# Kernel tuning notes

Measured on AMD Instinct MI355X. Metric: run time of the kernel, lower is better.

The kernel has to match this reference:

```python
import jax, jax.numpy as jnp
import numpy as np

B, S, D, N, L, V = 2, 512, 1024, 4096, 4, 32000
EPS = 1e-5

def ternarize(w):
    # BitNet b1.58-style: scale = mean |w|, quantize to {-1,0,1}, rescale.
    s = jnp.mean(jnp.abs(w)) + 1e-8
    return s * jnp.round(jnp.clip(w / s, -1.0, 1.0))

def tern_ste(w):
    # straight-through estimator (faithful to ternary training)
    return w + jax.lax.stop_gradient(ternarize(w) - w)

def layer_norm(x, g, b):
    mu = jnp.mean(x, axis=-1, keepdims=True)
    var = jnp.var(x, axis=-1, keepdims=True)
    return (x - mu) * jax.lax.rsqrt(var + EPS) * g + b

def setup_inputs() -> dict:
    key = jax.random.key(0)
    ks = jax.random.split(key, 20)
    sc = lambda d: 1.0 / np.sqrt(d)
    inp = {
        'input_ids': jax.random.randint(ks[0], (B, S), 0, V, dtype=jnp.int32),
        'emb':       jax.random.normal(ks[1], (V, D), jnp.float32) * 0.02,
        'pos_emb':   jax.random.normal(ks[2], (S, D), jnp.float32) * 0.02,
        'gru_wih':   jax.random.normal(ks[3], (3 * D, D), jnp.float32) * sc(D),
        'gru_whh':   jax.random.normal(ks[4], (3 * D, D), jnp.float32) * sc(D),
        'gru_bih':   jnp.zeros((3 * D,), jnp.float32),
        'gru_bhh':   jnp.zeros((3 * D,), jnp.float32),
        'syn_w':     jax.random.normal(ks[5], (L, N, D), jnp.float32) * sc(D),
        'syn_b':     jnp.zeros((L, N), jnp.float32),
        'out_w':     jax.random.normal(ks[6], (L, D, N), jnp.float32) * sc(N),
        'out_b':     jnp.zeros((L, D), jnp.float32),
        'ln_g':      jnp.ones((L, D), jnp.float32),
        'ln_b':      jnp.zeros((L, D), jnp.float32),
        'on_g':      jnp.ones((D,), jnp.float32),
        'on_b':      jnp.zeros((D,), jnp.float32),
        'head_w':    jax.random.normal(ks[7], (V, D), jnp.float32) * sc(D),
        'head_b':    jnp.zeros((V,), jnp.float32),
    }
    return inp

def gru(x, wih, whh, bih, bhh):
    # x: [B,S,D] -> [B,S,D], torch nn.GRU semantics, h0 = 0
    # Precompute input projections for all timesteps: [B,S,3D]
    gi_all = jnp.einsum('bsd,ed->bse', x, wih) + bih
    def step(h, gi):
        gh = h @ whh.T + bhh
        ir, iz, inn = jnp.split(gi, 3, axis=-1)
        hr, hz, hn = jnp.split(gh, 3, axis=-1)
        r = jax.nn.sigmoid(ir + hr)
        z = jax.nn.sigmoid(iz + hz)
        n = jnp.tanh(inn + r * hn)
        h_new = (1.0 - z) * n + z * h
        return h_new, h_new
    h0 = jnp.zeros((x.shape[0], whh.shape[1]), x.dtype)
    _, hs = jax.lax.scan(step, h0, jnp.swapaxes(gi_all, 0, 1))
    return jnp.swapaxes(hs, 0, 1)

def reference(input_ids, emb, pos_emb, gru_wih, gru_whh, gru_bih, gru_bhh,
              syn_w, syn_b, out_w, out_b, ln_g, ln_b, on_g, on_b,
              head_w, head_b):
    # Ternary embedding lookup
    x = tern_ste(emb)[input_ids]                       # [B,S,D]
    x = x + pos_emb[None, :x.shape[1], :]
    x = gru(x, gru_wih, gru_whh, gru_bih, gru_bhh)
    for l in range(L):
        residual = x
        hidden = jax.nn.relu(jnp.einsum('bsd,nd->bsn', x, tern_ste(syn_w[l])) + syn_b[l])
        out = jnp.einsum('bsn,dn->bsd', hidden, tern_ste(out_w[l])) + out_b[l]
        x = layer_norm(residual + out, ln_g[l], ln_b[l])
    x = layer_norm(x, on_g, on_b)
    logits = jnp.einsum('bsd,vd->bsv', x, tern_ste(head_w)) + head_b  # [B,S,V]
    return logits
```

## Files before the change

kernel.cpp:

```cpp
#include <hip/hip_runtime.h>
#include <hip/hip_bf16.h>
#include <cstdint>
#include <cstddef>

#define Dm 1024
#define Sm 512
#define Bm 2
#define Nm 4096
#define Lm 4
#define Vm 32000

typedef __attribute__((ext_vector_type(8))) short short8;
typedef __attribute__((ext_vector_type(4))) float floatx4;

__device__ __forceinline__ unsigned short f2b(float f){
  union { float f; unsigned u; } v; v.f = f;
  unsigned r = (v.u + 0x7fffu + ((v.u >> 16) & 1u)) >> 16;
  return (unsigned short)r;
}
__device__ __forceinline__ float b2f(unsigned short h){
  union { unsigned u; float f; } v; v.u = ((unsigned)h) << 16;
  return v.f;
}

__device__ __forceinline__ void gload16(const unsigned short* g, unsigned short* l){
  __builtin_amdgcn_global_load_lds(
      (const __attribute__((address_space(1))) void*)g,
      (__attribute__((address_space(3))) void*)l, 16, 0, 0);
}

__global__ __launch_bounds__(256) void absum_all_kernel(
    const float* __restrict__ emb, const float* __restrict__ syn_w,
    const float* __restrict__ out_w, const float* __restrict__ head_w,
    double* __restrict__ partial)
{
  int wid = blockIdx.x >> 7;
  int blk = blockIdx.x & 127;
  const float* base; long n4;
  if (wid == 0){ base = emb; n4 = (long)Vm * Dm / 4; }
  else if (wid <= 4){ base = syn_w + (size_t)(wid - 1) * Nm * Dm; n4 = (long)Nm * Dm / 4; }
  else if (wid <= 8){ base = out_w + (size_t)(wid - 5) * Dm * Nm; n4 = (long)Nm * Dm / 4; }
  else { base = head_w; n4 = (long)Vm * Dm / 4; }

  long i = (long)blk * 256 + threadIdx.x;
  const long stride = 128L * 256;
  double s = 0.0;
  for (; i < n4; i += stride){
    float4 v = ((const float4*)base)[i];
    s += (double)fabsf(v.x) + (double)fabsf(v.y) + (double)fabsf(v.z) + (double)fabsf(v.w);
  }
  #pragma unroll
  for (int off = 32; off; off >>= 1) s += __shfl_down(s, off, 64);
  __shared__ double wsum[4];
  int lane = threadIdx.x & 63, wv = threadIdx.x >> 6;
  if (lane == 0) wsum[wv] = s;
  __syncthreads();
  if (threadIdx.x == 0) partial[wid * 128 + blk] = wsum[0] + wsum[1] + wsum[2] + wsum[3];
}

__global__ __launch_bounds__(128) void scale_kernel(const double* __restrict__ partials,
                                                    float* __restrict__ scales){
  int b = blockIdx.x;
  int tid = threadIdx.x;
  __shared__ double red[128];
  red[tid] = partials[b * 128 + tid];
  __syncthreads();
  for (int off = 64; off; off >>= 1){
    if (tid < off) red[tid] += red[tid + off];
    __syncthreads();
  }
  if (tid == 0){
    double cnt = (b == 0 || b == 9) ? (double)Vm * (double)Dm : (double)Nm * (double)Dm;
    scales[b] = (float)(red[0] / cnt);
  }
}

__global__ __launch_bounds__(256) void tern_kernel(const float* __restrict__ w,
                                                   const float* __restrict__ smean,
                                                   unsigned short* __restrict__ out, long n4){
  float s = smean[0] + 1e-8f;
  long i = (long)blockIdx.x * blockDim.x + threadIdx.x;
  long stride = (long)gridDim.x * blockDim.x;
  for (; i < n4; i += stride){
    float4 v = ((const float4*)w)[i];
    ushort4 o;
    o.x = f2b(rintf(fminf(fmaxf(v.x / s, -1.f), 1.f)));
    o.y = f2b(rintf(fminf(fmaxf(v.y / s, -1.f), 1.f)));
    o.z = f2b(rintf(fminf(fmaxf(v.z / s, -1.f), 1.f)));
    o.w = f2b(rintf(fminf(fmaxf(v.w / s, -1.f), 1.f)));
    ((ushort4*)out)[i] = o;
  }
}

__global__ __launch_bounds__(256) void split_kernel(const float* __restrict__ w,
                                                    unsigned short* __restrict__ hi,
                                                    unsigned short* __restrict__ lo, long n4){
  long i = (long)blockIdx.x * blockDim.x + threadIdx.x;
  long stride = (long)gridDim.x * blockDim.x;
  for (; i < n4; i += stride){
    float4 v = ((const float4*)w)[i];
    float f[4] = {v.x, v.y, v.z, v.w};
    ushort4 h4, l4;
    unsigned short* hp = (unsigned short*)&h4;
    unsigned short* lp = (unsigned short*)&l4;
    #pragma unroll
    for (int e = 0; e < 4; e++){
      unsigned short h = f2b(f[e]);
      hp[e] = h;
      lp[e] = f2b(f[e] - b2f(h));
    }
    ((ushort4*)hi)[i] = h4;
    ((ushort4*)lo)[i] = l4;
  }
}

__global__ __launch_bounds__(256) void embed_kernel(
    const int* __restrict__ ids, const float* __restrict__ emb,
    const float* __restrict__ pos, const float* __restrict__ smean,
    unsigned short* __restrict__ xhi, unsigned short* __restrict__ xlo)
{
  int row = blockIdx.x;
  int sp  = row & (Sm - 1);
  int id  = ids[row];
  float s = smean[0] + 1e-8f;
  int d = threadIdx.x * 4;
  float4 wv = *(const float4*)(emb + (size_t)id * Dm + d);
  float4 pv = *(const float4*)(pos + (size_t)sp * Dm + d);
  float y[4];
  y[0] = s * rintf(fminf(fmaxf(wv.x / s, -1.f), 1.f)) + pv.x;
  y[1] = s * rintf(fminf(fmaxf(wv.y / s, -1.f), 1.f)) + pv.y;
  y[2] = s * rintf(fminf(fmaxf(wv.z / s, -1.f), 1.f)) + pv.z;
  y[3] = s * rintf(fminf(fmaxf(wv.w / s, -1.f), 1.f)) + pv.w;
  ushort4 h4, l4;
  unsigned short* hp = (unsigned short*)&h4;
  unsigned short* lp = (unsigned short*)&l4;
  #pragma unroll
  for (int e = 0; e < 4; e++){
    unsigned short h = f2b(y[e]);
    hp[e] = h;
    lp[e] = f2b(y[e] - b2f(h));
  }
  size_t base = (size_t)row * Dm + d;
  *(ushort4*)(xhi + base) = h4;
  *(ushort4*)(xlo + base) = l4;
}

template<bool WSPLIT, bool WF32, int BT>
__global__ __launch_bounds__(256) void gemm_kernel(
    const unsigned short* __restrict__ Ahi, const unsigned short* __restrict__ Alo,
    const void* __restrict__ Wsrc, const unsigned short* __restrict__ Wlo,
    const float* __restrict__ bias, const float* __restrict__ smean,
    int relu, float* __restrict__ outf,
    unsigned short* __restrict__ outhi, unsigned short* __restrict__ outlo,
    int M, int N, int K)
{
  constexpr int WT = BT / 2;
  constexpr int FT = WT / 16;
  constexpr int RPT = 256 / BT;
  constexpr int CPT = 32 / RPT;
  constexpr int NU  = CPT / 8;

  __shared__ unsigned short As[2][BT][40];
  __shared__ unsigned short Bs[WSPLIT ? 2 : 1][BT][40];
  int tid = threadIdx.x;
  int wave = tid >> 6, lane = tid & 63;
  int wm = wave >> 1, wn = wave & 1;
  int bm = blockIdx.y, bn = blockIdx.x;

  bool tern = (smean != nullptr);
  float s = 1.f;
  if (tern) s = smean[0] + 1e-8f;

  int arow = tid / RPT, sub = tid % RPT;
  int col0 = sub * CPT;
  const unsigned short* Agh = Ahi + (size_t)(bm * BT + arow) * K + col0;
  const unsigned short* Agl = Alo + (size_t)(bm * BT + arow) * K + col0;
  const float* Wgf = nullptr;
  const unsigned short* Wgh = nullptr;
  const unsigned short* Wgl = nullptr;
  if (WF32) Wgf = (const float*)Wsrc + (size_t)(bn * BT + arow) * K + col0;
  else {
    Wgh = (const unsigned short*)Wsrc + (size_t)(bn * BT + arow) * K + col0;
    if (WSPLIT) Wgl = Wlo + (size_t)(bn * BT + arow) * K + col0;
  }

  floatx4 acc[FT][FT];
  #pragma unroll
  for (int i = 0; i < FT; i++)
    #pragma unroll
    for (int j = 0; j < FT; j++)
      acc[i][j] = (floatx4){0.f, 0.f, 0.f, 0.f};

  int kpb = K / (int)gridDim.z;
  int k_beg = blockIdx.z * kpb;

  for (int k0 = k_beg; k0 < k_beg + kpb; k0 += 32){
    __syncthreads();
    #pragma unroll
    for (int u = 0; u < NU; u++){
      *(uint4*)&As[0][arow][col0 + u * 8] = *(const uint4*)(Agh + k0 + u * 8);
      *(uint4*)&As[1][arow][col0 + u * 8] = *(const uint4*)(Agl + k0 + u * 8);
    }
    if (WF32){
      unsigned short tmp[CPT];
      #pragma unroll
      for (int q = 0; q < CPT / 4; q++){
        float4 wv = *(const float4*)(Wgf + k0 + q * 4);
        float f[4] = {wv.x, wv.y, wv.z, wv.w};
        #pragma unroll
        for (int e = 0; e < 4; e++){
          float w = f[e];
          if (tern) w = rintf(fminf(fmaxf(w / s, -1.f), 1.f));
          tmp[q * 4 + e] = f2b(w);
        }
      }
      #pragma unroll
      for (int u = 0; u < NU; u++)
        *(uint4*)&Bs[0][arow][col0 + u * 8] = *(uint4*)&tmp[u * 8];
    } else {
      #pragma unroll
      for (int u = 0; u < NU; u++){
        *(uint4*)&Bs[0][arow][col0 + u * 8] = *(const uint4*)(Wgh + k0 + u * 8);
        if (WSPLIT)
          *(uint4*)&Bs[1][arow][col0 + u * 8] = *(const uint4*)(Wgl + k0 + u * 8);
      }
    }
    __syncthreads();

    int kq = lane >> 4, mr = lane & 15;
    short8 afh[FT], afl[FT], bfh[FT];
    #pragma unroll
    for (int i = 0; i < FT; i++){
      afh[i] = *(const short8*)&As[0][wm*WT + i*16 + mr][kq*8];
      afl[i] = *(const short8*)&As[1][wm*WT + i*16 + mr][kq*8];
    }
    #pragma unroll
    for (int j = 0; j < FT; j++) bfh[j] = *(const short8*)&Bs[0][wn*WT + j*16 + mr][kq*8];
    #pragma unroll
    for (int i = 0; i < FT; i++)
      #pragma unroll
      for (int j = 0; j < FT; j++){
        acc[i][j] = __builtin_amdgcn_mfma_f32_16x16x32_bf16(afh[i], bfh[j], acc[i][j], 0, 0, 0);
        acc[i][j] = __builtin_amdgcn_mfma_f32_16x16x32_bf16(afl[i], bfh[j], acc[i][j], 0, 0, 0);
      }
    if (WSPLIT){
      short8 bfl[FT];
      #pragma unroll
      for (int j = 0; j < FT; j++) bfl[j] = *(const short8*)&Bs[1][wn*WT + j*16 + mr][kq*8];
      #pragma unroll
      for (int i = 0; i < FT; i++)
        #pragma unroll
        for (int j = 0; j < FT; j++)
          acc[i][j] = __builtin_amdgcn_mfma_f32_16x16x32_bf16(afh[i], bfl[j], acc[i][j], 0, 0, 0);
    }
  }

  bool split = (gridDim.z > 1);
  bool addb = (blockIdx.z == 0);
  int cr = lane >> 4, cc = lane & 15;
  #pragma unroll
  for (int j = 0; j < FT; j++){
    int col = bn * BT + wn * WT + j * 16 + cc;
    float bv = (bias && addb) ? bias[col] : 0.f;
    #pragma unroll
    for (int i = 0; i < FT; i++){
      #pragma unroll
      for (int r = 0; r < 4; r++){
        int row = bm * BT + wm * WT + i * 16 + cr * 4 + r;
        float v = acc[i][j][r] * s + bv;
        if (relu) v = fmaxf(v, 0.f);
        size_t idx = (size_t)row * N + col;
        if (outf){
          if (split) atomicAdd(outf + idx, v);
          else outf[idx] = v;
        }
        if (outhi){
          unsigned short h = f2b(v);
          outhi[idx] = h;
          outlo[idx] = f2b(v - b2f(h));
        }
      }
    }
  }
}

__global__ __launch_bounds__(256) void gemm_lds_kernel(
    const unsigned short* __restrict__ Ahi, const unsigned short* __restrict__ Alo,
    const unsigned short* __restrict__ Whi,
    const float* __restrict__ bias, const float* __restrict__ smean,
    int relu, float* __restrict__ outf, int M, int N, int K)
{
  __shared__ __align__(16) unsigned short lds[3 * 4096];
  int tid = threadIdx.x;
  int wave = tid >> 6, lane = tid & 63;
  int wm = wave >> 1, wn = wave & 1;
  int bm = blockIdx.y, bn = blockIdx.x;

  float s = 1.f;
  if (smean) s = smean[0] + 1e-8f;

  int r0 = wave * 32 + (lane >> 2);
  int r1 = r0 + 16;
  int s0 = (lane & 3) ^ ((r0 >> 1) & 3);
  int s1 = (lane & 3) ^ ((r1 >> 1) & 3);
  const unsigned short* ga0 = Ahi + (size_t)(bm * 128 + r0) * K + s0 * 8;
  const unsigned short* ga1 = Ahi + (size_t)(bm * 128 + r1) * K + s1 * 8;
  const unsigned short* gl0 = Alo + (size_t)(bm * 128 + r0) * K + s0 * 8;
  const unsigned short* gl1 = Alo + (size_t)(bm * 128 + r1) * K + s1 * 8;
  const unsigned short* gw0 = Whi + (size_t)(bn * 128 + r0) * K + s0 * 8;
  const unsigned short* gw1 = Whi + (size_t)(bn * 128 + r1) * K + s1 * 8;
  unsigned short* la = &lds[wave * 1024];

  floatx4 acc[4][4];
  #pragma unroll
  for (int i = 0; i < 4; i++)
    #pragma unroll
    for (int j = 0; j < 4; j++)
      acc[i][j] = (floatx4){0.f, 0.f, 0.f, 0.f};

  for (int k0 = 0; k0 < K; k0 += 32){
    __syncthreads();
    gload16(ga0 + k0, la);
    gload16(ga1 + k0, la + 512);
    gload16(gl0 + k0, la + 4096);
    gload16(gl1 + k0, la + 4096 + 512);
    gload16(gw0 + k0, la + 8192);
    gload16(gw1 + k0, la + 8192 + 512);
    __syncthreads();

    int kq = lane >> 4, mr = lane & 15;
    short8 afh[4], afl[4], bfh[4];
    #pragma unroll
    for (int i = 0; i < 4; i++){
      int r = wm * 64 + i * 16 + mr;
      int off = r * 32 + ((kq ^ ((r >> 1) & 3)) << 3);
      afh[i] = *(const short8*)&lds[off];
      afl[i] = *(const short8*)&lds[4096 + off];
    }
    #pragma unroll
    for (int j = 0; j < 4; j++){
      int r = wn * 64 + j * 16 + mr;
      int off = r * 32 + ((kq ^ ((r >> 1) & 3)) << 3);
      bfh[j] = *(const short8*)&lds[8192 + off];
    }
    #pragma unroll
    for (int i = 0; i < 4; i++)
      #pragma unroll
      for (int j = 0; j < 4; j++){
        acc[i][j] = __builtin_amdgcn_mfma_f32_16x16x32_bf16(afh[i], bfh[j], acc[i][j], 0, 0, 0);
        acc[i][j] = __builtin_amdgcn_mfma_f32_16x16x32_bf16(afl[i], bfh[j], acc[i][j], 0, 0, 0);
      }
  }

  int cr = lane >> 4, cc = lane & 15;
  #pragma unroll
  for (int j = 0; j < 4; j++){
    int col = bn * 128 + wn * 64 + j * 16 + cc;
    float bv = bias ? bias[col] : 0.f;
    #pragma unroll
    for (int i = 0; i < 4; i++){
      #pragma unroll
      for (int r = 0; r < 4; r++){
        int row = bm * 128 + wm * 64 + i * 16 + cr * 4 + r;
        float v = acc[i][j][r] * s + bv;
        if (relu) v = fmaxf(v, 0.f);
        outf[(size_t)row * N + col] = v;
      }
    }
  }
}

__global__ __launch_bounds__(1024) void gru_kernel(
    const float* __restrict__ gi, const float* __restrict__ whh, const float* __restrict__ bhh,
    unsigned long long* __restrict__ hbuf, float* __restrict__ hs,
    unsigned short* __restrict__ xhi, unsigned short* __restrict__ xlo)
{
  __shared__ float lds_h[2 * 1088];
  __shared__ float lds_gh[96];
  int w = blockIdx.x, tid = threadIdx.x;
  int d0 = w * 16;
  int o = tid >> 4, c = tid & 15;
  bool active = (o < 48);
  int g = o >> 4, dl = o & 15;
  int wrow = g * Dm + d0 + dl;
  float wreg[64];
  if (active){
    const float* src = whh + (size_t)wrow * Dm + c * 64;
    #pragma unroll
    for (int i = 0; i < 64; i++) wreg[i] = src[i];
  }
  float bhval = active ? bhh[wrow] : 0.f;

  int bb = tid >> 4, dd = tid & 15;
  float hprev = 0.f;

  for (int t = 0; t < Sm; t++){
    float ir = 0.f, iz = 0.f, inn = 0.f;
    if (tid < 32){
      const float* girow = gi + ((size_t)bb * Sm + t) * (3 * Dm);
      int d = d0 + dd;
      ir  = girow[d];
      iz  = girow[Dm + d];
      inn = girow[2 * Dm + d];
    }
    {
      const unsigned long long* src = hbuf + (size_t)(t & 1) * 2048 + tid * 2;
      unsigned got = 0;
      int spins = 0;
      while (got != 3u){
        #pragma unroll
        for (int q = 0; q < 2; q++){
          if (!(got & (1u << q))){
            unsigned long long wd = __hip_atomic_load(src + q, __ATOMIC_RELAXED,
                                                      __HIP_MEMORY_SCOPE_AGENT);
            if ((unsigned)(wd >> 32) == (unsigned)t){
              union { unsigned u; float f; } cv; cv.u = (unsigned)wd;
              int wi = tid * 2 + q;
              int b = wi >> 10, d = wi & 1023;
              lds_h[b * 1088 + (d >> 6) * 68 + (d & 63)] = cv.f;
              got |= 1u << q;
            }
          }
        }
        if (got != 3u){
          if (++spins > (1 << 20)) break;
          __builtin_amdgcn_s_sleep(1);
        }
      }
    }
    __syncthreads();
    if (active){
      const float* hp = lds_h + c * 68;
      float a0 = 0.f, a1 = 0.f;
      #pragma unroll
      for (int i = 0; i < 64; i++){
        float wv = wreg[i];
        a0 += wv * hp[i];
        a1 += wv * hp[1088 + i];
      }
      #pragma unroll
      for (int off = 8; off; off >>= 1){
        a0 += __shfl_xor(a0, off, 16);
        a1 += __shfl_xor(a1, off, 16);
      }
      if (c == 0){
        lds_gh[o]      = a0 + bhval;
        lds_gh[48 + o] = a1 + bhval;
      }
    }
    __syncthreads();
    if (tid < 32){
      float gr = lds_gh[bb * 48 + dd];
      float gz = lds_gh[bb * 48 + 16 + dd];
      float gn = lds_gh[bb * 48 + 32 + dd];
      float rr = 1.f / (1.f + expf(-(ir + gr)));
      float zz = 1.f / (1.f + expf(-(iz + gz)));
      float nn = tanhf(inn + rr * gn);
      float hnew = (1.f - zz) * nn + zz * hprev;
      hprev = hnew;
      int d = d0 + dd;
      union { float f; unsigned u; } cv; cv.f = hnew;
      unsigned long long wd = ((unsigned long long)(unsigned)(t + 1) << 32) | (unsigned long long)cv.u;
      __hip_atomic_store(hbuf + (size_t)((t + 1) & 1) * 2048 + bb * Dm + d, wd,
                         __ATOMIC_RELAXED, __HIP_MEMORY_SCOPE_AGENT);
      size_t oi = ((size_t)bb * Sm + t) * Dm + d;
      hs[oi] = hnew;
      unsigned short h = f2b(hnew);
      xhi[oi] = h;
      xlo[oi] = f2b(hnew - b2f(h));
    }
  }
}

__global__ __launch_bounds__(256) void ln_kernel(
    const float* __restrict__ resid, const float* __restrict__ addv,
    const float* __restrict__ g, const float* __restrict__ b,
    float* __restrict__ outf, unsigned short* __restrict__ outhi,
    unsigned short* __restrict__ outlo)
{
  int row = blockIdx.x;
  int d = threadIdx.x * 4;
  size_t base = (size_t)row * Dm + d;
  float4 v = *(const float4*)(resid + base);
  if (addv){
    float4 a = *(const float4*)(addv + base);
    v.x += a.x; v.y += a.y; v.z += a.z; v.w += a.w;
  }
  float sum = v.x + v.y + v.z + v.w;
  float sq  = v.x*v.x + v.y*v.y + v.z*v.z + v.w*v.w;
  #pragma unroll
  for (int off = 32; off; off >>= 1){
    sum += __shfl_down(sum, off, 64);
    sq  += __shfl_down(sq,  off, 64);
  }
  __shared__ float red[4][2];
  __shared__ float bc[2];
  int lane = threadIdx.x & 63, wv = threadIdx.x >> 6;
  if (lane == 0){ red[wv][0] = sum; red[wv][1] = sq; }
  __syncthreads();
  if (threadIdx.x == 0){
    float st = red[0][0] + red[1][0] + red[2][0] + red[3][0];
    float qt = red[0][1] + red[1][1] + red[2][1] + red[3][1];
    float mu = st * (1.f / Dm);
    float var = qt * (1.f / Dm) - mu * mu;
    bc[0] = mu; bc[1] = rsqrtf(var + 1e-5f);
  }
  __syncthreads();
  float mu = bc[0], rs = bc[1];
  float4 gv = *(const float4*)(g + d);
  float4 bv = *(const float4*)(b + d);
  float y[4];
  y[0] = (v.x - mu) * rs * gv.x + bv.x;
  y[1] = (v.y - mu) * rs * gv.y + bv.y;
  y[2] = (v.z - mu) * rs * gv.z + bv.z;
  y[3] = (v.w - mu) * rs * gv.w + bv.w;
  if (outf) *(float4*)(outf + base) = *(float4*)y;
  if (outhi){
    ushort4 h4, l4;
    unsigned short* hp = (unsigned short*)&h4;
    unsigned short* lp = (unsigned short*)&l4;
    #pragma unroll
    for (int e = 0; e < 4; e++){
      unsigned short h = f2b(y[e]);
      hp[e] = h;
      lp[e] = f2b(y[e] - b2f(h));
    }
    *(ushort4*)(outhi + base) = h4;
    *(ushort4*)(outlo + base) = l4;
  }
}

extern "C" void kernel_launch(void* const* d_in, const int* in_sizes, int n_in,
                              void* d_out, int out_size, void* d_ws, size_t ws_size,
                              hipStream_t stream)
{
  const int*   ids    = (const int*)  d_in[0];
  const float* emb    = (const float*)d_in[1];
  const float* pos    = (const float*)d_in[2];
  const float* wih    = (const float*)d_in[3];
  const float* whh    = (const float*)d_in[4];
  const float* bih    = (const float*)d_in[5];
  const float* bhh    = (const float*)d_in[6];
  const float* syn_w  = (const float*)d_in[7];
  const float* syn_b  = (const float*)d_in[8];
  const float* out_w  = (const float*)d_in[9];
  const float* out_b  = (const float*)d_in[10];
  const float* ln_g   = (const float*)d_in[11];
  const float* ln_b   = (const float*)d_in[12];
  const float* on_g   = (const float*)d_in[13];
  const float* on_b   = (const float*)d_in[14];
  const float* head_w = (const float*)d_in[15];
  const float* head_b = (const float*)d_in[16];
  float* logits = (float*)d_out;

  const size_t MB = (size_t)1 << 20;
  char* ws = (char*)d_ws;
  float*  scales   = (float*) ws;
  double* partials = (double*)(ws + 32768);
  unsigned long long* hbuf = (unsigned long long*)(ws + 131072);
  float*          hs     = (float*)         (ws + 1  * MB);
  unsigned short* xhi    = (unsigned short*)(ws + 5  * MB);
  unsigned short* xlo    = (unsigned short*)(ws + 7  * MB);
  float*          outbuf = (float*)         (ws + 9  * MB);
  float*          gi     = (float*)         (ws + 13 * MB);
  unsigned short* wih_hi = (unsigned short*)(ws + 25 * MB);
  unsigned short* wih_lo = (unsigned short*)(ws + 31 * MB);
  unsigned short* hhi    = (unsigned short*)(ws + 37 * MB);
  unsigned short* hlo    = (unsigned short*)(ws + 45 * MB);
  unsigned short* wbuf   = (unsigned short*)(ws + 53 * MB);

  bool pre_layer = ws_size >= 62  * MB;
  bool pre_head  = ws_size >= 120 * MB;

  hipMemsetAsync(d_ws, 0, 163840, stream);

  absum_all_kernel<<<1280, 256, 0, stream>>>(emb, syn_w, out_w, head_w, partials);
  scale_kernel<<<10, 128, 0, stream>>>(partials, scales);

  embed_kernel<<<1024, 256, 0, stream>>>(ids, emb, pos, scales, xhi, xlo);

  split_kernel<<<2048, 256, 0, stream>>>(wih, wih_hi, wih_lo, (long)(3 * Dm) * Dm / 4);
  gemm_kernel<true, false, 64><<<dim3(3072/64, 1024/64, 1), 256, 0, stream>>>(
      xhi, xlo, wih_hi, wih_lo, bih, nullptr, 0, gi, nullptr, nullptr, 1024, 3072, 1024);

  gru_kernel<<<64, 1024, 0, stream>>>(gi, whh, bhh, hbuf, hs, xhi, xlo);

  for (int l = 0; l < Lm; l++){
    if (pre_layer){
      tern_kernel<<<2048, 256, 0, stream>>>(syn_w + (size_t)l * Nm * Dm, scales + 1 + l,
                                            wbuf, (long)Nm * Dm / 4);
      gemm_kernel<false, false, 64><<<dim3(4096/64, 1024/64, 1), 256, 0, stream>>>(
          xhi, xlo, wbuf, nullptr, syn_b + (size_t)l * Nm, scales + 1 + l,
          1, nullptr, hhi, hlo, 1024, 4096, 1024);
    } else {
      gemm_kernel<false, true, 64><<<dim3(4096/64, 1024/64, 1), 256, 0, stream>>>(
          xhi, xlo, syn_w + (size_t)l * Nm * Dm, nullptr, syn_b + (size_t)l * Nm, scales + 1 + l,
          1, nullptr, hhi, hlo, 1024, 4096, 1024);
    }
    hipMemsetAsync(outbuf, 0, (size_t)1024 * 1024 * 4, stream);
    if (pre_layer){
      tern_kernel<<<2048, 256, 0, stream>>>(out_w + (size_t)l * Dm * Nm, scales + 5 + l,
                                            wbuf, (long)Dm * Nm / 4);
      gemm_kernel<false, false, 64><<<dim3(1024/64, 1024/64, 2), 256, 0, stream>>>(
          hhi, hlo, wbuf, nullptr, out_b + (size_t)l * Dm, scales + 5 + l,
          0, outbuf, nullptr, nullptr, 1024, 1024, 4096);
    } else {
      gemm_kernel<false, true, 64><<<dim3(1024/64, 1024/64, 2), 256, 0, stream>>>(
          hhi, hlo, out_w + (size_t)l * Dm * Nm, nullptr, out_b + (size_t)l * Dm, scales + 5 + l,
          0, outbuf, nullptr, nullptr, 1024, 1024, 4096);
    }
    ln_kernel<<<1024, 256, 0, stream>>>(hs, outbuf, ln_g + (size_t)l * Dm, ln_b + (size_t)l * Dm,
                                        hs, xhi, xlo);
  }
  ln_kernel<<<1024, 256, 0, stream>>>(hs, nullptr, on_g, on_b, nullptr, xhi, xlo);

  if (pre_head){
    tern_kernel<<<2048, 256, 0, stream>>>(head_w, scales + 9, wbuf, (long)Vm * Dm / 4);
    gemm_lds_kernel<<<dim3(32000/128, 1024/128, 1), 256, 0, stream>>>(
        xhi, xlo, wbuf, head_b, scales + 9, 0, logits, 1024, 32000, 1024);
  } else {
    gemm_kernel<false, true, 128><<<dim3(32000/128, 1024/128, 1), 256, 0, stream>>>(
        xhi, xlo, head_w, nullptr, head_b, scales + 9, 0, logits, nullptr, nullptr, 1024, 32000, 1024);
  }
}
```

Baseline: 2.170 ms.

## Restructure GRU step: one wave per hidden unit, double-buffered LDS, single barrier

```diff
diff --git a/kernel.cpp b/kernel.cpp
--- a/kernel.cpp
+++ b/kernel.cpp
@@ -375,36 +375,41 @@
     unsigned long long* __restrict__ hbuf, float* __restrict__ hs,
     unsigned short* __restrict__ xhi, unsigned short* __restrict__ xlo)
 {
-  __shared__ float lds_h[2 * 1088];
-  __shared__ float lds_gh[96];
+  __shared__ float lds_h[2][2][1024];
   int w = blockIdx.x, tid = threadIdx.x;
   int d0 = w * 16;
-  int o = tid >> 4, c = tid & 15;
-  bool active = (o < 48);
-  int g = o >> 4, dl = o & 15;
-  int wrow = g * Dm + d0 + dl;
-  float wreg[64];
-  if (active){
-    const float* src = whh + (size_t)wrow * Dm + c * 64;
-    #pragma unroll
-    for (int i = 0; i < 64; i++) wreg[i] = src[i];
-  }
-  float bhval = active ? bhh[wrow] : 0.f;
-
-  int bb = tid >> 4, dd = tid & 15;
-  float hprev = 0.f;
+  int dl = tid >> 6;
+  int c  = tid & 63;
+  int d  = d0 + dl;
+
+  float wreg[3][16];
+  #pragma unroll
+  for (int g = 0; g < 3; g++){
+    const float* src = whh + (size_t)(g * Dm + d) * Dm + c * 16;
+    #pragma unroll
+    for (int q = 0; q < 4; q++){
+      float4 v = *(const float4*)(src + q * 4);
+      wreg[g][q*4+0] = v.x; wreg[g][q*4+1] = v.y;
+      wreg[g][q*4+2] = v.z; wreg[g][q*4+3] = v.w;
+    }
+  }
+  float bh[3];
+  #pragma unroll
+  for (int g = 0; g < 3; g++) bh[g] = bhh[g * Dm + d];
+
+  float hprev0 = 0.f, hprev1 = 0.f;
 
   for (int t = 0; t < Sm; t++){
-    float ir = 0.f, iz = 0.f, inn = 0.f;
-    if (tid < 32){
-      const float* girow = gi + ((size_t)bb * Sm + t) * (3 * Dm);
-      int d = d0 + dd;
-      ir  = girow[d];
-      iz  = girow[Dm + d];
-      inn = girow[2 * Dm + d];
+    float ir0=0.f, iz0=0.f, in0=0.f, ir1=0.f, iz1=0.f, in1=0.f;
+    if (c == 0){
+      const float* g0 = gi + (size_t)t * (3 * Dm);
+      const float* g1 = gi + ((size_t)Sm + t) * (3 * Dm);
+      ir0 = g0[d]; iz0 = g0[Dm + d]; in0 = g0[2*Dm + d];
+      ir1 = g1[d]; iz1 = g1[Dm + d]; in1 = g1[2*Dm + d];
     }
     {
       const unsigned long long* src = hbuf + (size_t)(t & 1) * 2048 + tid * 2;
+      float* ldst = &lds_h[t & 1][0][0];
       unsigned got = 0;
       int spins = 0;
       while (got != 3u){
@@ -416,58 +421,66 @@
             if ((unsigned)(wd >> 32) == (unsigned)t){
               union { unsigned u; float f; } cv; cv.u = (unsigned)wd;
               int wi = tid * 2 + q;
-              int b = wi >> 10, d = wi & 1023;
-              lds_h[b * 1088 + (d >> 6) * 68 + (d & 63)] = cv.f;
+              int b = wi >> 10, dv = wi & 1023;
+              ldst[b * 1024 + ((dv >> 2) & 3) * 256 + (dv >> 4) * 4 + (dv & 3)] = cv.f;
               got |= 1u << q;
             }
           }
         }
         if (got != 3u){
-          if (++spins > (1 << 20)) break;
+          if (++spins > (1 << 18)) break;
           __builtin_amdgcn_s_sleep(1);
         }
       }
     }
     __syncthreads();
-    if (active){
-      const float* hp = lds_h + c * 68;
-      float a0 = 0.f, a1 = 0.f;
-      #pragma unroll
-      for (int i = 0; i < 64; i++){
-        float wv = wreg[i];
-        a0 += wv * hp[i];
-        a1 += wv * hp[1088 + i];
-      }
-      #pragma unroll
-      for (int off = 8; off; off >>= 1){
-        a0 += __shfl_xor(a0, off, 16);
-        a1 += __shfl_xor(a1, off, 16);
-      }
-      if (c == 0){
-        lds_gh[o]      = a0 + bhval;
-        lds_gh[48 + o] = a1 + bhval;
-      }
-    }
-    __syncthreads();
-    if (tid < 32){
-      float gr = lds_gh[bb * 48 + dd];
-      float gz = lds_gh[bb * 48 + 16 + dd];
-      float gn = lds_gh[bb * 48 + 32 + dd];
-      float rr = 1.f / (1.f + expf(-(ir + gr)));
-      float zz = 1.f / (1.f + expf(-(iz + gz)));
-      float nn = tanhf(inn + rr * gn);
-      float hnew = (1.f - zz) * nn + zz * hprev;
-      hprev = hnew;
-      int d = d0 + dd;
-      union { float f; unsigned u; } cv; cv.f = hnew;
-      unsigned long long wd = ((unsigned long long)(unsigned)(t + 1) << 32) | (unsigned long long)cv.u;
-      __hip_atomic_store(hbuf + (size_t)((t + 1) & 1) * 2048 + bb * Dm + d, wd,
-                         __ATOMIC_RELAXED, __HIP_MEMORY_SCOPE_AGENT);
-      size_t oi = ((size_t)bb * Sm + t) * Dm + d;
-      hs[oi] = hnew;
-      unsigned short h = f2b(hnew);
-      xhi[oi] = h;
-      xlo[oi] = f2b(hnew - b2f(h));
+    float acc[3][2] = {{0.f,0.f},{0.f,0.f},{0.f,0.f}};
+    const float* hp = &lds_h[t & 1][0][0];
+    #pragma unroll
+    for (int b = 0; b < 2; b++){
+      #pragma unroll
+      for (int q = 0; q < 4; q++){
+        float4 hv = *(const float4*)&hp[b * 1024 + q * 256 + c * 4];
+        #pragma unroll
+        for (int g = 0; g < 3; g++){
+          acc[g][b] += wreg[g][q*4+0] * hv.x;
+          acc[g][b] += wreg[g][q*4+1] * hv.y;
+          acc[g][b] += wreg[g][q*4+2] * hv.z;
+          acc[g][b] += wreg[g][q*4+3] * hv.w;
+        }
+      }
+    }
+    #pragma unroll
+    for (int off = 32; off; off >>= 1){
+      #pragma unroll
+      for (int g = 0; g < 3; g++){
+        acc[g][0] += __shfl_xor(acc[g][0], off, 64);
+        acc[g][1] += __shfl_xor(acc[g][1], off, 64);
+      }
+    }
+    if (c == 0){
+      float gr0 = acc[0][0] + bh[0], gz0 = acc[1][0] + bh[1], gn0 = acc[2][0] + bh[2];
+      float gr1 = acc[0][1] + bh[0], gz1 = acc[1][1] + bh[1], gn1 = acc[2][1] + bh[2];
+      float rr0 = 1.f / (1.f + expf(-(ir0 + gr0)));
+      float zz0 = 1.f / (1.f + expf(-(iz0 + gz0)));
+      float nn0 = tanhf(in0 + rr0 * gn0);
+      float h0 = (1.f - zz0) * nn0 + zz0 * hprev0;
+      float rr1 = 1.f / (1.f + expf(-(ir1 + gr1)));
+      float zz1 = 1.f / (1.f + expf(-(iz1 + gz1)));
+      float nn1 = tanhf(in1 + rr1 * gn1);
+      float h1 = (1.f - zz1) * nn1 + zz1 * hprev1;
+      hprev0 = h0; hprev1 = h1;
+      unsigned long long* dst = hbuf + (size_t)((t + 1) & 1) * 2048;
+      union { float f; unsigned u; } cv0, cv1; cv0.f = h0; cv1.f = h1;
+      unsigned long long tag = (unsigned long long)(unsigned)(t + 1) << 32;
+      __hip_atomic_store(dst + d,        tag | cv0.u, __ATOMIC_RELAXED, __HIP_MEMORY_SCOPE_AGENT);
+      __hip_atomic_store(dst + 1024 + d, tag | cv1.u, __ATOMIC_RELAXED, __HIP_MEMORY_SCOPE_AGENT);
+      size_t oi0 = (size_t)t * Dm + d;
+      size_t oi1 = ((size_t)Sm + t) * Dm + d;
+      hs[oi0] = h0; hs[oi1] = h1;
+      unsigned short hh0 = f2b(h0), hh1 = f2b(h1);
+      xhi[oi0] = hh0; xlo[oi0] = f2b(h0 - b2f(hh0));
+      xhi[oi1] = hh1; xlo[oi1] = f2b(h1 - b2f(hh1));
     }
   }
 }
```

Result: slower. 3.293 ms (+51.8%).
